# Kernel tuning notes

Measured on AMD Instinct MI355X. Metric: run time of the kernel, lower is better.

Reference implementation:

```python
import jax, jax.numpy as jnp
import numpy as np

NEG = -9e15
ALPHA = 0.2  # leaky_relu negative slope


def setup_inputs() -> dict:
    key = jax.random.key(0)
    k1, k2, k3, k4, k5 = jax.random.split(key, 5)
    N, F_in, F_out = 8192, 128, 128
    x = jax.random.normal(k1, (N, F_in), dtype=jnp.float32)
    adj = jax.random.randint(k2, (N, N), 0, 2).astype(jnp.float32)
    # xavier-ish scaled params
    W = jax.random.normal(k3, (F_in, F_out), dtype=jnp.float32) * (1.0 / np.sqrt(F_in))
    a1 = jax.random.normal(k4, (F_out,), dtype=jnp.float32) * (1.0 / np.sqrt(2 * F_out))
    a2 = jax.random.normal(k5, (F_out,), dtype=jnp.float32) * (1.0 / np.sqrt(2 * F_out))
    a_bias = jnp.zeros((1,), dtype=jnp.float32)
    return {"x": x, "adj": adj, "W": W, "a1": a1, "a2": a2, "a_bias": a_bias}


def reference(x, adj, W, a1, a2, a_bias):
    # h = W(input)                                   [N, F]
    h = x @ W
    # a(concat(h_i, h_j)) == h_i.a1 + h_j.a2 + b  -> avoids N*N*2F concat
    s1 = h @ a1  # [N]
    s2 = h @ a2  # [N]
    e = jax.nn.leaky_relu(s1[:, None] + s2[None, :] + a_bias[0], negative_slope=ALPHA)  # [N, N]
    e = jnp.where(adj > 0, e, NEG)
    attention = jax.nn.softmax(e, axis=1)
    # dropout p=0 (deterministic eval): identity
    return attention @ h
```

## Files before the change

### kernel.cpp

```cpp
#include <hip/hip_runtime.h>
#include <hip/hip_bf16.h>

typedef __attribute__((ext_vector_type(8)))  __bf16         bf16x8;
typedef __attribute__((ext_vector_type(4)))  float          f32x4;
typedef __attribute__((ext_vector_type(8)))  unsigned short u16x8;

#define LOG2E 1.44269504088896340736f

#if __has_builtin(__builtin_amdgcn_exp2f)
#define EXP2F(x) __builtin_amdgcn_exp2f(x)
#else
#define EXP2F(x) __builtin_exp2f(x)
#endif

__device__ __forceinline__ unsigned short f2b(float f) {
  union { __bf16 h; unsigned short s; } o; o.h = (__bf16)f; return o.s;
}

__global__ __launch_bounds__(256) void k_prep(
    const float* __restrict__ x, const float* __restrict__ W,
    const float* __restrict__ a1, const float* __restrict__ a2,
    const float* __restrict__ ab,
    unsigned short* __restrict__ hT, float* __restrict__ s1p,
    float* __restrict__ s2p) {
  __shared__ __align__(16) float Ws[64 * 128];
  __shared__ __align__(16) float Xs[16 * 128];
  const int t = threadIdx.x;
  const int rb = blockIdx.x * 16;
  const int r  = t >> 4;
  const int fg = t & 15;

  {
    int off = t * 8;
    *(f32x4*)(Xs + off)     = *(const f32x4*)(x + (long)rb * 128 + off);
    *(f32x4*)(Xs + off + 4) = *(const f32x4*)(x + (long)rb * 128 + off + 4);
  }

  float acc[8];
#pragma unroll
  for (int j = 0; j < 8; ++j) acc[j] = 0.f;

  for (int half = 0; half < 2; ++half) {
    __syncthreads();
#pragma unroll
    for (int c = 0; c < 8; ++c) {
      int off = c * 1024 + t * 4;
      *(f32x4*)(Ws + off) = *(const f32x4*)(W + half * 8192 + off);
    }
    __syncthreads();
    for (int k = 0; k < 64; ++k) {
      float xv = Xs[r * 128 + half * 64 + k];
      f32x4 w0 = *(const f32x4*)(Ws + k * 128 + fg * 8);
      f32x4 w1 = *(const f32x4*)(Ws + k * 128 + fg * 8 + 4);
#pragma unroll
      for (int j = 0; j < 4; ++j) {
        acc[j]     += xv * w0[j];
        acc[4 + j] += xv * w1[j];
      }
    }
  }

  float p1 = 0.f, p2 = 0.f;
#pragma unroll
  for (int j = 0; j < 8; ++j) {
    p1 += acc[j] * a1[fg * 8 + j];
    p2 += acc[j] * a2[fg * 8 + j];
  }
#pragma unroll
  for (int mask = 1; mask <= 8; mask <<= 1) {
    p1 += __shfl_xor(p1, mask, 64);
    p2 += __shfl_xor(p2, mask, 64);
  }
  if (fg == 0) {
    s1p[rb + r] = LOG2E * (p1 + ab[0]);
    s2p[rb + r] = LOG2E * p2;
  }
#pragma unroll
  for (int j = 0; j < 8; ++j)
    hT[(long)(fg * 8 + j) * 8192 + rb + r] = f2b(acc[j]);
}

__global__ __launch_bounds__(512, 4) void k_attn(
    const float* __restrict__ adj, const unsigned short* __restrict__ hT,
    const float* __restrict__ s1p, const float* __restrict__ s2p,
    float* __restrict__ out) {
  __shared__ __align__(16) unsigned short Bs[128 * 128];
  __shared__ __align__(16) unsigned short As[16 * 136];
  __shared__ float dens[16];

  const int t = threadIdx.x;
  const int i0 = blockIdx.x * 16;
  const int lane = t & 63;
  const int wv = t >> 6;
  const int m    = lane & 15;
  const int quad = lane >> 4;
  const int f0 = wv * 16;

  const int wr = t >> 5;
  const int wc = t & 31;
  const int sf    = t >> 4;
  const int sslot = t & 15;

  const float s1v = s1p[i0 + wr];
  const float* adjp = adj + (long)(i0 + wr) * 8192 + wc * 4;
  const float* s2pp = s2p + wc * 4;

  f32x4 acc;
#pragma unroll
  for (int p = 0; p < 4; ++p) acc[p] = 0.f;
  float den = 0.f;

  f32x4 ar = __builtin_nontemporal_load((const f32x4*)(adjp));
  f32x4 cs = *(const f32x4*)(s2pp);
  u16x8 stg[4];
#pragma unroll
  for (int rr = 0; rr < 4; ++rr) {
    int f = rr * 32 + sf;
    int cg = sslot ^ (f & 7);
    stg[rr] = *(const u16x8*)(hT + (long)f * 8192 + cg * 8);
  }

  for (int it = 0; it < 64; ++it) {
#pragma unroll
    for (int rr = 0; rr < 4; ++rr) {
      int f = rr * 32 + sf;
      *(u16x8*)(Bs + f * 128 + sslot * 8) = stg[rr];
    }
    const int itn = (it + 1) & 63;
    f32x4 nr = __builtin_nontemporal_load((const f32x4*)(adjp + (long)itn * 128));
    f32x4 ns = *(const f32x4*)(s2pp + itn * 128);

    {
      ushort4 w;
      float dloc = 0.f;
      float tp0 = s1v + cs[0];
      float tp1 = s1v + cs[1];
      float tp2 = s1v + cs[2];
      float tp3 = s1v + cs[3];
      float w0 = ar[0] * EXP2F(fmaxf(tp0, 0.2f * tp0));
      float w1 = ar[1] * EXP2F(fmaxf(tp1, 0.2f * tp1));
      float w2 = ar[2] * EXP2F(fmaxf(tp2, 0.2f * tp2));
      float w3 = ar[3] * EXP2F(fmaxf(tp3, 0.2f * tp3));
      dloc = (w0 + w1) + (w2 + w3);
      w.x = f2b(w0); w.y = f2b(w1); w.z = f2b(w2); w.w = f2b(w3);
      den += dloc;
      *(ushort4*)(As + wr * 136 + wc * 4) = w;
    }

    __syncthreads();

    if (it < 63) {
      const unsigned short* hTi = hT + (long)(it + 1) * 128;
#pragma unroll
      for (int rr = 0; rr < 4; ++rr) {
        int f = rr * 32 + sf;
        int cg = sslot ^ (f & 7);
        stg[rr] = *(const u16x8*)(hTi + (long)f * 8192 + cg * 8);
      }
    }

#pragma unroll
    for (int ks = 0; ks < 4; ++ks) {
      bf16x8 af = *(const bf16x8*)(As + m * 136 + ks * 32 + quad * 8);
      int slotx = (ks * 4 + quad) ^ ((f0 + m) & 7);
      bf16x8 bv = *(const bf16x8*)(Bs + (f0 + m) * 128 + slotx * 8);
      acc = __builtin_amdgcn_mfma_f32_16x16x32_bf16(af, bv, acc, 0, 0, 0);
    }
    __syncthreads();

    ar = nr; cs = ns;
  }

  den += __shfl_xor(den, 1, 64);
  den += __shfl_xor(den, 2, 64);
  den += __shfl_xor(den, 4, 64);
  den += __shfl_xor(den, 8, 64);
  den += __shfl_xor(den, 16, 64);
  if (wc == 0) dens[wr] = den;
  __syncthreads();

#pragma unroll
  for (int p = 0; p < 4; ++p) {
    int row = quad * 4 + p;
    float d = dens[row];
    float inv = (d != 0.f) ? (1.f / d) : 0.f;
    out[(long)(i0 + row) * 128 + f0 + m] = acc[p] * inv;
  }
}

extern "C" void kernel_launch(void* const* d_in, const int* in_sizes, int n_in,
                              void* d_out, int out_size, void* d_ws, size_t ws_size,
                              hipStream_t stream) {
  int ix = 0, iadj = 1, iw = 2, ia1 = 3, ia2 = 4, iab = 5;
  {
    int f128[2] = {-1, -1};
    int tx = -1, tadj = -1, tw = -1, tab = -1, n128 = 0;
    for (int i = 0; i < n_in; ++i) {
      int s = in_sizes[i];
      if (s == 67108864) tadj = i;
      else if (s == 1048576) tx = i;
      else if (s == 16384) tw = i;
      else if (s == 128 && n128 < 2) f128[n128++] = i;
      else if (s == 1) tab = i;
    }
    if (tx >= 0 && tadj >= 0 && tw >= 0 && tab >= 0 && n128 == 2) {
      ix = tx; iadj = tadj; iw = tw; ia1 = f128[0]; ia2 = f128[1]; iab = tab;
    }
  }
  const float* x   = (const float*)d_in[ix];
  const float* adj = (const float*)d_in[iadj];
  const float* W   = (const float*)d_in[iw];
  const float* a1  = (const float*)d_in[ia1];
  const float* a2  = (const float*)d_in[ia2];
  const float* ab  = (const float*)d_in[iab];

  char* ws = (char*)d_ws;
  unsigned short* hT = (unsigned short*)(ws);
  float* s1p = (float*)(ws + 2097152);
  float* s2p = (float*)(ws + 2097152 + 32768);

  k_prep<<<dim3(512), dim3(256), 0, stream>>>(x, W, a1, a2, ab, hT, s1p, s2p);
  k_attn<<<dim3(512), dim3(512), 0, stream>>>(adj, hT, s1p, s2p, (float*)d_out);
}
```

Before: 397.5 us.

## Restructure attention kernel to split-K across two waves with register-resident fragments

The attention kernel moves from 512-thread blocks that stage h and attention weights through LDS with two barriers per step to 128-thread blocks. Each of the two waves handles half of the key dimension for all 128 output features, and attention weights are built directly in MFMA A-fragment registers. B fragments are loaded straight from global memory, with a single LDS reduction of the two partial results at the end. This drops the per-iteration LDS traffic and synchronization, but each block now has far fewer waves and hT is read uncoalesced and redundantly from global/L2. With only 1024 waves in total, hiding memory latency on the adj stream may be harder.

```diff
diff --git a/kernel.cpp b/kernel.cpp
--- a/kernel.cpp
+++ b/kernel.cpp
@@ -3,7 +3,6 @@
 
 typedef __attribute__((ext_vector_type(8)))  __bf16         bf16x8;
 typedef __attribute__((ext_vector_type(4)))  float          f32x4;
-typedef __attribute__((ext_vector_type(8)))  unsigned short u16x8;
 
 #define LOG2E 1.44269504088896340736f
 
@@ -80,13 +79,12 @@
     hT[(long)(fg * 8 + j) * 8192 + rb + r] = f2b(acc[j]);
 }
 
-__global__ __launch_bounds__(512, 4) void k_attn(
+__global__ __launch_bounds__(128) void k_attn(
     const float* __restrict__ adj, const unsigned short* __restrict__ hT,
     const float* __restrict__ s1p, const float* __restrict__ s2p,
     float* __restrict__ out) {
-  __shared__ __align__(16) unsigned short Bs[128 * 128];
-  __shared__ __align__(16) unsigned short As[16 * 136];
-  __shared__ float dens[16];
+  __shared__ float accL[16 * 128];
+  __shared__ float denL[16];
 
   const int t = threadIdx.x;
   const int i0 = blockIdx.x * 16;
@@ -94,97 +92,96 @@
   const int wv = t >> 6;
   const int m    = lane & 15;
   const int quad = lane >> 4;
-  const int f0 = wv * 16;
-
-  const int wr = t >> 5;
-  const int wc = t & 31;
-  const int sf    = t >> 4;
-  const int sslot = t & 15;
-
-  const float s1v = s1p[i0 + wr];
-  const float* adjp = adj + (long)(i0 + wr) * 8192 + wc * 4;
-  const float* s2pp = s2p + wc * 4;
-
-  f32x4 acc;
-#pragma unroll
-  for (int p = 0; p < 4; ++p) acc[p] = 0.f;
+  const long kbase = (long)wv * 4096;
+
+  const float s1v = s1p[i0 + m];
+  const float* adjp = adj + (long)(i0 + m) * 8192 + kbase + quad * 8;
+  const float* s2pp = s2p + kbase + quad * 8;
+  const unsigned short* hTq = hT + kbase + quad * 8;
+
+  f32x4 acc[8];
+#pragma unroll
+  for (int ft = 0; ft < 8; ++ft)
+#pragma unroll
+    for (int p = 0; p < 4; ++p) acc[ft][p] = 0.f;
   float den = 0.f;
 
-  f32x4 ar = __builtin_nontemporal_load((const f32x4*)(adjp));
-  f32x4 cs = *(const f32x4*)(s2pp);
-  u16x8 stg[4];
-#pragma unroll
-  for (int rr = 0; rr < 4; ++rr) {
-    int f = rr * 32 + sf;
-    int cg = sslot ^ (f & 7);
-    stg[rr] = *(const u16x8*)(hT + (long)f * 8192 + cg * 8);
-  }
-
-  for (int it = 0; it < 64; ++it) {
-#pragma unroll
-    for (int rr = 0; rr < 4; ++rr) {
-      int f = rr * 32 + sf;
-      *(u16x8*)(Bs + f * 128 + sslot * 8) = stg[rr];
-    }
-    const int itn = (it + 1) & 63;
-    f32x4 nr = __builtin_nontemporal_load((const f32x4*)(adjp + (long)itn * 128));
-    f32x4 ns = *(const f32x4*)(s2pp + itn * 128);
-
-    {
-      ushort4 w;
-      float dloc = 0.f;
-      float tp0 = s1v + cs[0];
-      float tp1 = s1v + cs[1];
-      float tp2 = s1v + cs[2];
-      float tp3 = s1v + cs[3];
-      float w0 = ar[0] * EXP2F(fmaxf(tp0, 0.2f * tp0));
-      float w1 = ar[1] * EXP2F(fmaxf(tp1, 0.2f * tp1));
-      float w2 = ar[2] * EXP2F(fmaxf(tp2, 0.2f * tp2));
-      float w3 = ar[3] * EXP2F(fmaxf(tp3, 0.2f * tp3));
-      dloc = (w0 + w1) + (w2 + w3);
-      w.x = f2b(w0); w.y = f2b(w1); w.z = f2b(w2); w.w = f2b(w3);
-      den += dloc;
-      *(ushort4*)(As + wr * 136 + wc * 4) = w;
-    }
-
-    __syncthreads();
-
-    if (it < 63) {
-      const unsigned short* hTi = hT + (long)(it + 1) * 128;
-#pragma unroll
-      for (int rr = 0; rr < 4; ++rr) {
-        int f = rr * 32 + sf;
-        int cg = sslot ^ (f & 7);
-        stg[rr] = *(const u16x8*)(hTi + (long)f * 8192 + cg * 8);
-      }
-    }
-
+  f32x4 ca[4][2];
+#pragma unroll
+  for (int ks = 0; ks < 4; ++ks) {
+    ca[ks][0] = __builtin_nontemporal_load((const f32x4*)(adjp + ks * 32));
+    ca[ks][1] = __builtin_nontemporal_load((const f32x4*)(adjp + ks * 32 + 4));
+  }
+
+  for (int it = 0; it < 32; ++it) {
+    f32x4 na[4][2];
+    if (it < 31) {
+      const float* ap = adjp + (long)(it + 1) * 128;
+#pragma unroll
+      for (int ks = 0; ks < 4; ++ks) {
+        na[ks][0] = __builtin_nontemporal_load((const f32x4*)(ap + ks * 32));
+        na[ks][1] = __builtin_nontemporal_load((const f32x4*)(ap + ks * 32 + 4));
+      }
+    }
+
+    bf16x8 afr[4];
 #pragma unroll
     for (int ks = 0; ks < 4; ++ks) {
-      bf16x8 af = *(const bf16x8*)(As + m * 136 + ks * 32 + quad * 8);
-      int slotx = (ks * 4 + quad) ^ ((f0 + m) & 7);
-      bf16x8 bv = *(const bf16x8*)(Bs + (f0 + m) * 128 + slotx * 8);
-      acc = __builtin_amdgcn_mfma_f32_16x16x32_bf16(af, bv, acc, 0, 0, 0);
-    }
-    __syncthreads();
-
-    ar = nr; cs = ns;
-  }
-
-  den += __shfl_xor(den, 1, 64);
-  den += __shfl_xor(den, 2, 64);
-  den += __shfl_xor(den, 4, 64);
-  den += __shfl_xor(den, 8, 64);
+      const float* sp = s2pp + (long)it * 128 + ks * 32;
+      f32x4 sv0 = *(const f32x4*)(sp);
+      f32x4 sv1 = *(const f32x4*)(sp + 4);
+#pragma unroll
+      for (int j = 0; j < 4; ++j) {
+        float tp0 = s1v + sv0[j];
+        float w0 = ca[ks][0][j] * EXP2F(fmaxf(tp0, 0.2f * tp0));
+        den += w0;
+        afr[ks][j] = (__bf16)w0;
+        float tp1 = s1v + sv1[j];
+        float w1 = ca[ks][1][j] * EXP2F(fmaxf(tp1, 0.2f * tp1));
+        den += w1;
+        afr[ks][4 + j] = (__bf16)w1;
+      }
+    }
+
+    const unsigned short* hb = hTq + (long)it * 128;
+#pragma unroll
+    for (int ks = 0; ks < 4; ++ks) {
+#pragma unroll
+      for (int ft = 0; ft < 8; ++ft) {
+        bf16x8 bv = *(const bf16x8*)(hb + (long)(ft * 16 + m) * 8192 + ks * 32);
+        acc[ft] = __builtin_amdgcn_mfma_f32_16x16x32_bf16(afr[ks], bv, acc[ft], 0, 0, 0);
+      }
+    }
+
+#pragma unroll
+    for (int ks = 0; ks < 4; ++ks) { ca[ks][0] = na[ks][0]; ca[ks][1] = na[ks][1]; }
+  }
+
   den += __shfl_xor(den, 16, 64);
-  if (wc == 0) dens[wr] = den;
+  den += __shfl_xor(den, 32, 64);
+
+  if (wv == 1) {
+    if (lane < 16) denL[lane] = den;
+#pragma unroll
+    for (int ft = 0; ft < 8; ++ft)
+#pragma unroll
+      for (int p = 0; p < 4; ++p)
+        accL[(quad * 4 + p) * 128 + ft * 16 + m] = acc[ft][p];
+  }
   __syncthreads();
-
-#pragma unroll
-  for (int p = 0; p < 4; ++p) {
-    int row = quad * 4 + p;
-    float d = dens[row];
-    float inv = (d != 0.f) ? (1.f / d) : 0.f;
-    out[(long)(i0 + row) * 128 + f0 + m] = acc[p] * inv;
+  if (wv == 0) {
+    float dtot = den + denL[m];
+#pragma unroll
+    for (int p = 0; p < 4; ++p) {
+      int row = quad * 4 + p;
+      float dr = __shfl(dtot, (lane & 0x30) | row, 64);
+      float inv = (dr != 0.f) ? (1.f / dr) : 0.f;
+#pragma unroll
+      for (int ft = 0; ft < 8; ++ft) {
+        float v = acc[ft][p] + accL[row * 128 + ft * 16 + m];
+        out[(long)(i0 + row) * 128 + ft * 16 + m] = v * inv;
+      }
+    }
   }
 }
 
@@ -220,5 +217,5 @@
   float* s2p = (float*)(ws + 2097152 + 32768);
 
   k_prep<<<dim3(512), dim3(256), 0, stream>>>(x, W, a1, a2, ab, hT, s1p, s2p);
-  k_attn<<<dim3(512), dim3(512), 0, stream>>>(adj, hT, s1p, s2p, (float*)d_out);
-}
+  k_attn<<<dim3(512), dim3(128), 0, stream>>>(adj, hT, s1p, s2p, (float*)d_out);
+}
```

Measured after the change: 600.0 us. 1.51x slower.

## Split K across wave halves, load B operands directly from global, double-buffer A

Applied to the files above, without the earlier changes.

The attention kernel now splits the 8192 key dimension into two halves handled by separate groups of four waves. Each wave computes a 16x32 output tile, and the two partial accumulators and denominators are reduced through shared memory at the end. The hT (B operand) tile is no longer staged in LDS: MFMA operands are read straight from global/L2. The attention weight tile is double-buffered so each iteration needs only one barrier, and adjacency loads are prefetched two steps ahead. The aim is to cut LDS traffic and barrier count and get more memory overlap. The trade-off is more scattered global reads of hT and extra shared memory for the final reduction.

```diff
diff --git a/kernel.cpp b/kernel.cpp
--- a/kernel.cpp
+++ b/kernel.cpp
@@ -3,7 +3,6 @@
 
 typedef __attribute__((ext_vector_type(8)))  __bf16         bf16x8;
 typedef __attribute__((ext_vector_type(4)))  float          f32x4;
-typedef __attribute__((ext_vector_type(8)))  unsigned short u16x8;
 
 #define LOG2E 1.44269504088896340736f
 
@@ -84,107 +83,124 @@
     const float* __restrict__ adj, const unsigned short* __restrict__ hT,
     const float* __restrict__ s1p, const float* __restrict__ s2p,
     float* __restrict__ out) {
-  __shared__ __align__(16) unsigned short Bs[128 * 128];
-  __shared__ __align__(16) unsigned short As[16 * 136];
-  __shared__ float dens[16];
+  __shared__ __align__(16) unsigned short Abuf[2][2][16 * 128];
+  __shared__ float accC[16 * 128];
+  __shared__ float dens[2][16];
 
   const int t = threadIdx.x;
   const int i0 = blockIdx.x * 16;
+  const int wh = t >> 8;
+  const int wr = (t >> 4) & 15;
+  const int wc = t & 15;
   const int lane = t & 63;
   const int wv = t >> 6;
+  const int kh = wv >> 2;
+  const int f0 = (wv & 3) * 32;
   const int m    = lane & 15;
   const int quad = lane >> 4;
-  const int f0 = wv * 16;
-
-  const int wr = t >> 5;
-  const int wc = t & 31;
-  const int sf    = t >> 4;
-  const int sslot = t & 15;
 
   const float s1v = s1p[i0 + wr];
-  const float* adjp = adj + (long)(i0 + wr) * 8192 + wc * 4;
-  const float* s2pp = s2p + wc * 4;
-
-  f32x4 acc;
-#pragma unroll
-  for (int p = 0; p < 4; ++p) acc[p] = 0.f;
+  const float* adjp = adj + (long)(i0 + wr) * 8192 + wh * 4096 + wc * 8;
+  const float* s2pp = s2p + wh * 4096 + wc * 8;
+  const unsigned short* hTb = hT + (long)kh * 4096 + quad * 8;
+  unsigned short* Aw = &Abuf[0][0][0] + wh * 2048;
+  const unsigned short* Ar = &Abuf[0][0][0] + kh * 2048;
+  const int wslot = (wc ^ (wr & 7)) * 8;
+
+  f32x4 acc0, acc1;
+#pragma unroll
+  for (int p = 0; p < 4; ++p) { acc0[p] = 0.f; acc1[p] = 0.f; }
   float den = 0.f;
 
-  f32x4 ar = __builtin_nontemporal_load((const f32x4*)(adjp));
-  f32x4 cs = *(const f32x4*)(s2pp);
-  u16x8 stg[4];
-#pragma unroll
-  for (int rr = 0; rr < 4; ++rr) {
-    int f = rr * 32 + sf;
-    int cg = sslot ^ (f & 7);
-    stg[rr] = *(const u16x8*)(hT + (long)f * 8192 + cg * 8);
-  }
-
-  for (int it = 0; it < 64; ++it) {
-#pragma unroll
-    for (int rr = 0; rr < 4; ++rr) {
-      int f = rr * 32 + sf;
-      *(u16x8*)(Bs + f * 128 + sslot * 8) = stg[rr];
-    }
-    const int itn = (it + 1) & 63;
-    f32x4 nr = __builtin_nontemporal_load((const f32x4*)(adjp + (long)itn * 128));
-    f32x4 ns = *(const f32x4*)(s2pp + itn * 128);
-
-    {
-      ushort4 w;
-      float dloc = 0.f;
-      float tp0 = s1v + cs[0];
-      float tp1 = s1v + cs[1];
-      float tp2 = s1v + cs[2];
-      float tp3 = s1v + cs[3];
-      float w0 = ar[0] * EXP2F(fmaxf(tp0, 0.2f * tp0));
-      float w1 = ar[1] * EXP2F(fmaxf(tp1, 0.2f * tp1));
-      float w2 = ar[2] * EXP2F(fmaxf(tp2, 0.2f * tp2));
-      float w3 = ar[3] * EXP2F(fmaxf(tp3, 0.2f * tp3));
-      dloc = (w0 + w1) + (w2 + w3);
-      w.x = f2b(w0); w.y = f2b(w1); w.z = f2b(w2); w.w = f2b(w3);
-      den += dloc;
-      *(ushort4*)(As + wr * 136 + wc * 4) = w;
-    }
-
+  {
+    f32x4 aa = __builtin_nontemporal_load((const f32x4*)(adjp));
+    f32x4 ab2 = __builtin_nontemporal_load((const f32x4*)(adjp + 4));
+    f32x4 sa = *(const f32x4*)(s2pp);
+    f32x4 sb = *(const f32x4*)(s2pp + 4);
+    bf16x8 wpk;
+#pragma unroll
+    for (int j = 0; j < 4; ++j) {
+      float tp0 = s1v + sa[j];
+      float w0 = aa[j] * EXP2F(fmaxf(tp0, 0.2f * tp0));
+      den += w0; wpk[j] = (__bf16)w0;
+      float tp1 = s1v + sb[j];
+      float w1 = ab2[j] * EXP2F(fmaxf(tp1, 0.2f * tp1));
+      den += w1; wpk[4 + j] = (__bf16)w1;
+    }
+    *(bf16x8*)(Aw + wr * 128 + wslot) = wpk;
+  }
+  f32x4 caa = __builtin_nontemporal_load((const f32x4*)(adjp + 128));
+  f32x4 cab = __builtin_nontemporal_load((const f32x4*)(adjp + 132));
+  f32x4 csa = *(const f32x4*)(s2pp + 128);
+  f32x4 csb = *(const f32x4*)(s2pp + 132);
+  __syncthreads();
+
+  for (int it = 0; it < 32; ++it) {
+    f32x4 naa, nab, nsa, nsb;
+    if (it + 2 < 32) {
+      const long o = (long)(it + 2) * 128;
+      naa = __builtin_nontemporal_load((const f32x4*)(adjp + o));
+      nab = __builtin_nontemporal_load((const f32x4*)(adjp + o + 4));
+      nsa = *(const f32x4*)(s2pp + o);
+      nsb = *(const f32x4*)(s2pp + o + 4);
+    }
+
+    if (it + 1 < 32) {
+      bf16x8 wpk;
+#pragma unroll
+      for (int j = 0; j < 4; ++j) {
+        float tp0 = s1v + csa[j];
+        float w0 = caa[j] * EXP2F(fmaxf(tp0, 0.2f * tp0));
+        den += w0; wpk[j] = (__bf16)w0;
+        float tp1 = s1v + csb[j];
+        float w1 = cab[j] * EXP2F(fmaxf(tp1, 0.2f * tp1));
+        den += w1; wpk[4 + j] = (__bf16)w1;
+      }
+      *(bf16x8*)(Aw + ((it + 1) & 1) * 4096 + wr * 128 + wslot) = wpk;
+    }
+
+    const unsigned short* Ac = Ar + (it & 1) * 4096 + m * 128;
+    const unsigned short* hb = hTb + (long)it * 128;
+#pragma unroll
+    for (int ks = 0; ks < 4; ++ks) {
+      int c = ks * 4 + quad;
+      bf16x8 af = *(const bf16x8*)(Ac + (c ^ (m & 7)) * 8);
+      bf16x8 bv0 = *(const bf16x8*)(hb + (long)(f0 + m) * 8192 + ks * 32);
+      bf16x8 bv1 = *(const bf16x8*)(hb + (long)(f0 + 16 + m) * 8192 + ks * 32);
+      acc0 = __builtin_amdgcn_mfma_f32_16x16x32_bf16(af, bv0, acc0, 0, 0, 0);
+      acc1 = __builtin_amdgcn_mfma_f32_16x16x32_bf16(af, bv1, acc1, 0, 0, 0);
+    }
     __syncthreads();
 
-    if (it < 63) {
-      const unsigned short* hTi = hT + (long)(it + 1) * 128;
-#pragma unroll
-      for (int rr = 0; rr < 4; ++rr) {
-        int f = rr * 32 + sf;
-        int cg = sslot ^ (f & 7);
-        stg[rr] = *(const u16x8*)(hTi + (long)f * 8192 + cg * 8);
-      }
-    }
-
-#pragma unroll
-    for (int ks = 0; ks < 4; ++ks) {
-      bf16x8 af = *(const bf16x8*)(As + m * 136 + ks * 32 + quad * 8);
-      int slotx = (ks * 4 + quad) ^ ((f0 + m) & 7);
-      bf16x8 bv = *(const bf16x8*)(Bs + (f0 + m) * 128 + slotx * 8);
-      acc = __builtin_amdgcn_mfma_f32_16x16x32_bf16(af, bv, acc, 0, 0, 0);
-    }
-    __syncthreads();
-
-    ar = nr; cs = ns;
+    caa = naa; cab = nab; csa = nsa; csb = nsb;
   }
 
   den += __shfl_xor(den, 1, 64);
   den += __shfl_xor(den, 2, 64);
   den += __shfl_xor(den, 4, 64);
   den += __shfl_xor(den, 8, 64);
-  den += __shfl_xor(den, 16, 64);
-  if (wc == 0) dens[wr] = den;
+  if (wc == 0) dens[wh][wr] = den;
+
+  if (kh == 1) {
+#pragma unroll
+    for (int p = 0; p < 4; ++p) {
+      int row = quad * 4 + p;
+      accC[row * 128 + f0 + m]      = acc0[p];
+      accC[row * 128 + f0 + 16 + m] = acc1[p];
+    }
+  }
   __syncthreads();
-
-#pragma unroll
-  for (int p = 0; p < 4; ++p) {
-    int row = quad * 4 + p;
-    float d = dens[row];
-    float inv = (d != 0.f) ? (1.f / d) : 0.f;
-    out[(long)(i0 + row) * 128 + f0 + m] = acc[p] * inv;
+  if (kh == 0) {
+#pragma unroll
+    for (int p = 0; p < 4; ++p) {
+      int row = quad * 4 + p;
+      float d = dens[0][row] + dens[1][row];
+      float inv = (d != 0.f) ? (1.f / d) : 0.f;
+      float v0 = acc0[p] + accC[row * 128 + f0 + m];
+      float v1 = acc1[p] + accC[row * 128 + f0 + 16 + m];
+      out[(long)(i0 + row) * 128 + f0 + m]      = v0 * inv;
+      out[(long)(i0 + row) * 128 + f0 + 16 + m] = v1 * inv;
+    }
   }
 }
 
```

New measurement: 467.0 us. +17.5%, slower.
